# Kernel optimization log

Hardware: AMD Instinct MI355X
Metric: run time of the kernel (lower is better)

## Reference

```python
import jax, jax.numpy as jnp
import numpy as np
import math

EMB_DIM = 256
HEADS = 8
HEAD_DIM = EMB_DIM // HEADS
N_LAYERS = 6
GRID_H = 32
GRID_W = 32
SEQ = GRID_H * GRID_W
LN_EPS = 1e-5


def _layernorm(x, w, b):
    mu = jnp.mean(x, axis=-1, keepdims=True)
    var = jnp.mean(jnp.square(x - mu), axis=-1, keepdims=True)
    return (x - mu) * jax.lax.rsqrt(var + LN_EPS) * w + b


def _sinusoidal_table(num_pos, dim):
    inv_freq = 1.0 / (10000.0 ** (jnp.arange(0, dim, 2, dtype=jnp.float32) / dim))
    t = jnp.arange(num_pos, dtype=jnp.float32)
    sinusoid = t[:, None] * inv_freq[None, :]  # [P, dim/2]
    return jnp.concatenate([jnp.sin(sinusoid), jnp.cos(sinusoid)], axis=-1)  # [P, dim]


def _alibi_bias(num_heads, seq_len):
    # 2D Manhattan distances over the flattened grid (Two-slope-Alibi: factors = 1)
    xs, ys = jnp.meshgrid(jnp.arange(GRID_H), jnp.arange(GRID_W), indexing='ij')
    xf = xs.reshape(-1).astype(jnp.float32)
    yf = ys.reshape(-1).astype(jnp.float32)
    dist = jnp.abs(xf[:, None] - xf[None, :]) + jnp.abs(yf[:, None] - yf[None, :])
    dist = jnp.abs(dist[:seq_len, :seq_len])  # rpe_abs=True
    i = jnp.arange(num_heads, dtype=jnp.float32)
    slopes_l = -(2.0 ** (-(1.0 + i)))   # start_exponent=1, geometric ratio 1/2, times -1
    slopes_r = -(2.0 ** (-(0.5 + i)))   # start_exponent=0.5
    alibi_l = slopes_l[:, None, None] * dist[None]
    alibi_r = slopes_r[:, None, None] * dist[None]
    # triu + tril (diagonal dist = 0 so double-count is harmless)
    return jnp.triu(alibi_r) + jnp.tril(alibi_l)  # [H, S, S]


def reference(tokens, pos_ids, emb_table, input_weight, position_weight,
              ln1_w, ln1_b, ln2_w, ln2_b, w1, b1, w2, b2, lnf_w, lnf_b):
    B, S = tokens.shape
    # embeddings + sinusoidal positional embedding, mixed via weighted_sum_no_norm
    x_emb = emb_table[tokens]                                   # [B, S, D]
    pos_emb = _sinusoidal_table(SEQ, EMB_DIM)[pos_ids][None]    # [1, S, D]
    x = input_weight * x_emb + position_weight * pos_emb        # [B, S, D]

    bias = _alibi_bias(HEADS, S)[None]                          # [1, H, S, S]
    scale = 1.0 / math.sqrt(HEAD_DIM)

    for l in range(N_LAYERS):
        # --- attention: manual 2D-Alibi path (q = k = v = layernormed x; no projections) ---
        xn = _layernorm(x, ln1_w[l], ln1_b[l])
        qkv = xn.reshape(B, S, HEADS, HEAD_DIM).transpose(0, 2, 1, 3)  # [B, H, S, d]
        scores = jnp.einsum('bhsd,bhtd->bhst', qkv, qkv) * scale + bias
        attn = jax.nn.softmax(scores, axis=-1)
        out = jnp.einsum('bhst,bhtd->bhsd', attn, qkv)
        out = out.transpose(0, 2, 1, 3).reshape(B, S, EMB_DIM)
        x = x + out
        # --- MLP: Linear(D, 2*mlp_dim) -> GELU(exact) -> Linear(2*mlp_dim, D) ---
        xn = _layernorm(x, ln2_w[l], ln2_b[l])
        h = jax.nn.gelu(xn @ w1[l] + b1[l], approximate=False)
        x = x + (h @ w2[l] + b2[l])

    return _layernorm(x, lnf_w, lnf_b)


def setup_inputs() -> dict:
    key = jax.random.key(0)
    ks = jax.random.split(key, 8)
    B, S, D, L = 16, SEQ, EMB_DIM, N_LAYERS
    H2 = 2 * 512  # mlp hidden = mlp_dim * 2
    return {
        'tokens': jax.random.randint(ks[0], (B, S), 0, 16),
        'pos_ids': jnp.arange(S),
        'emb_table': jax.random.normal(ks[1], (16, D), dtype=jnp.float32),
        'input_weight': jnp.ones((1,), jnp.float32),
        'position_weight': jnp.ones((1,), jnp.float32),
        'ln1_w': jnp.ones((L, D), jnp.float32),
        'ln1_b': jnp.zeros((L, D), jnp.float32),
        'ln2_w': jnp.ones((L, D), jnp.float32),
        'ln2_b': jnp.zeros((L, D), jnp.float32),
        'w1': jax.random.normal(ks[2], (L, D, H2), dtype=jnp.float32) * (1.0 / np.sqrt(D)),
        'b1': jnp.zeros((L, H2), jnp.float32),
        'w2': jax.random.normal(ks[3], (L, H2, D), dtype=jnp.float32) * (1.0 / np.sqrt(H2)),
        'b2': jnp.zeros((L, D), jnp.float32),
        'lnf_w': jnp.ones((D,), jnp.float32),
        'lnf_b': jnp.zeros((D,), jnp.float32),
    }
```

## Files before the change

### kernel.cpp

```cpp
#include <hip/hip_runtime.h>
#include <hip/hip_bf16.h>
#include <math.h>

#define B_   16
#define S_   1024
#define D_   256
#define H_   8
#define HD_  32
#define L_   6
#define H2_  1024
#define LN_EPS 1e-5f
#define LOG2E_ 1.4426950408889634f
#define SCALE_ 0.17677669529663687f

typedef __attribute__((ext_vector_type(8))) short frag;
typedef __attribute__((ext_vector_type(4))) float f32x4;

#define MFMA(a, b, c) __builtin_amdgcn_mfma_f32_16x16x32_bf16((a), (b), (c), 0, 0, 0)

__device__ inline ushort bf16b(float f) {
    uint u = __builtin_bit_cast(uint, f);
    u += 0x7fff + ((u >> 16) & 1);
    return (ushort)(u >> 16);
}
__device__ inline uint cvt_pk_bf16(float lo, float hi) {
    uint r;
    asm("v_cvt_pk_bf16_f32 %0, %1, %2" : "=v"(r) : "v"(lo), "v"(hi));
    return r;
}
__device__ inline float exp2_raw(float x) {
    float r;
    asm("v_exp_f32 %0, %1" : "=v"(r) : "v"(x));
    return r;
}
__device__ __forceinline__ void gload16(const ushort* g, ushort* l) {
    __builtin_amdgcn_global_load_lds(
        (const __attribute__((address_space(1))) uint*)g,
        (__attribute__((address_space(3))) uint*)l, 16, 0, 0);
}

__global__ __launch_bounds__(256) void wtr_kernel(
    const float* __restrict__ in, ushort* __restrict__ out, int K, int N)
{
    __shared__ ushort Ts[32][36];
    in  += (size_t)blockIdx.z * K * N;
    out += (size_t)blockIdx.z * K * N;
    int n0 = blockIdx.x * 32, k0 = blockIdx.y * 32;
    int r = threadIdx.x >> 3, c4 = (threadIdx.x & 7) * 4;
    float4 f = *(const float4*)(in + (size_t)(k0 + r) * N + n0 + c4);
    Ts[r][c4 + 0] = bf16b(f.x);
    Ts[r][c4 + 1] = bf16b(f.y);
    Ts[r][c4 + 2] = bf16b(f.z);
    Ts[r][c4 + 3] = bf16b(f.w);
    __syncthreads();
    ushort4 o = { Ts[c4 + 0][r], Ts[c4 + 1][r], Ts[c4 + 2][r], Ts[c4 + 3][r] };
    *(ushort4*)(out + (size_t)(n0 + r) * K + k0 + c4) = o;
}

__global__ __launch_bounds__(256) void embed_kernel(
    const int* __restrict__ tokens, const int* __restrict__ pos_ids,
    const float* __restrict__ emb, const float* __restrict__ iwp,
    const float* __restrict__ pwp, float* __restrict__ X)
{
    int bs = blockIdx.x;
    int s = bs & (S_ - 1);
    int d = threadIdx.x;
    int tok = tokens[bs];
    float p = (float)pos_ids[s];
    int j = (d < 128) ? d : (d - 128);
    float invf = exp2f(-(float)j * (13.287712379549449f / 128.0f));
    float ang = p * invf;
    float pe = (d < 128) ? sinf(ang) : cosf(ang);
    X[(size_t)bs * D_ + d] = iwp[0] * emb[tok * D_ + d] + pwp[0] * pe;
}

template<int MODE>
__global__ __launch_bounds__(256) void ln_kernel(
    const float* __restrict__ X, const float* __restrict__ w,
    const float* __restrict__ b, void* __restrict__ outp)
{
    int row = blockIdx.x * 4 + (threadIdx.x >> 6);
    int lane = threadIdx.x & 63;
    const float4 v = *(const float4*)(X + (size_t)row * D_ + lane * 4);
    float s = v.x + v.y + v.z + v.w;
    #pragma unroll
    for (int m = 1; m < 64; m <<= 1) s += __shfl_xor(s, m, 64);
    float mu = s * (1.0f / 256.0f);
    float dx = v.x - mu, dy = v.y - mu, dz = v.z - mu, dw = v.w - mu;
    float vs = dx * dx + dy * dy + dz * dz + dw * dw;
    #pragma unroll
    for (int m = 1; m < 64; m <<= 1) vs += __shfl_xor(vs, m, 64);
    float inv = rsqrtf(vs * (1.0f / 256.0f) + LN_EPS);
    float4 wv = *(const float4*)(w + lane * 4);
    float4 bv = *(const float4*)(b + lane * 4);
    float o0 = dx * inv * wv.x + bv.x;
    float o1 = dy * inv * wv.y + bv.y;
    float o2 = dz * inv * wv.z + bv.z;
    float o3 = dw * inv * wv.w + bv.w;
    if constexpr (MODE == 0) {
        float4 o = { o0, o1, o2, o3 };
        *(float4*)((float*)outp + (size_t)row * D_ + lane * 4) = o;
    } else {
        ushort4 o = { bf16b(o0), bf16b(o1), bf16b(o2), bf16b(o3) };
        *(ushort4*)((ushort*)outp + (size_t)row * D_ + lane * 4) = o;
    }
}

__global__ __launch_bounds__(256) void lnv_kernel(
    const float* __restrict__ X, const float* __restrict__ w,
    const float* __restrict__ b, ushort* __restrict__ XNB,
    ushort* __restrict__ VTI)
{
    __shared__ ushort Ts[64][264];
    const int blk = blockIdx.x;
    const int bb = blk >> 4;
    const int sblk = (blk & 15) * 64;
    const int wv = threadIdx.x >> 6, lane = threadIdx.x & 63;

    #pragma unroll
    for (int p = 0; p < 16; ++p) {
        int srow = p * 4 + wv;
        int row = bb * S_ + sblk + srow;
        const float4 v = *(const float4*)(X + (size_t)row * D_ + lane * 4);
        float s = v.x + v.y + v.z + v.w;
        #pragma unroll
        for (int m = 1; m < 64; m <<= 1) s += __shfl_xor(s, m, 64);
        float mu = s * (1.0f / 256.0f);
        float dx = v.x - mu, dy = v.y - mu, dz = v.z - mu, dw = v.w - mu;
        float vs = dx * dx + dy * dy + dz * dz + dw * dw;
        #pragma unroll
        for (int m = 1; m < 64; m <<= 1) vs += __shfl_xor(vs, m, 64);
        float inv = rsqrtf(vs * (1.0f / 256.0f) + LN_EPS);
        float4 wvv = *(const float4*)(w + lane * 4);
        float4 bvv = *(const float4*)(b + lane * 4);
        ushort4 o = { bf16b(dx * inv * wvv.x + bvv.x),
                      bf16b(dy * inv * wvv.y + bvv.y),
                      bf16b(dz * inv * wvv.z + bvv.z),
                      bf16b(dw * inv * wvv.w + bvv.w) };
        int h = lane >> 3, dd = (lane & 7) * 4;
        *(ushort4*)(XNB + (((size_t)(bb * H_ + h) * S_ + sblk + srow) * HD_ + dd)) = o;
        *(ushort4*)&Ts[srow][lane * 4] = o;
    }
    __syncthreads();

    const int h = threadIdx.x >> 5, d = threadIdx.x & 31;
    const int hd = threadIdx.x;
    ushort* dst = VTI + ((size_t)(bb * H_ + h) * HD_ + d) * S_ + sblk;
    #pragma unroll
    for (int c8 = 0; c8 < 8; ++c8) {
        uint4 o;
        uint tmp[4];
        #pragma unroll
        for (int pair = 0; pair < 4; ++pair) {
            int c0 = c8 * 8 + pair * 2;
            int c1 = c0 + 1;
            int t0 = 16 * (((c0 >> 5) & 1) + 2 * ((c0 >> 2) & 1)) + 4 * ((c0 >> 3) & 3) + (c0 & 3);
            int t1 = 16 * (((c1 >> 5) & 1) + 2 * ((c1 >> 2) & 1)) + 4 * ((c1 >> 3) & 3) + (c1 & 3);
            tmp[pair] = (uint)Ts[t0][hd] | ((uint)Ts[t1][hd] << 16);
        }
        o.x = tmp[0]; o.y = tmp[1]; o.z = tmp[2]; o.w = tmp[3];
        *(uint4*)(dst + c8 * 8) = o;
    }
}

__global__ __launch_bounds__(256) void attn_kernel(
    const ushort* __restrict__ XNB, const ushort* __restrict__ VTI,
    float* __restrict__ X)
{
    __shared__ ushort Kl[2][2048];
    __shared__ ushort Vl[2][2048];

    const int bi = blockIdx.x;
    const int xcd = bi & 7, m = bi >> 3;
    const int bh = xcd * 16 + (m >> 3);
    const int bx = m & 7;
    const int b = bh >> 3, h = bh & 7;

    const ushort* __restrict__ base = XNB + (size_t)bh * (S_ * HD_);
    const ushort* __restrict__ vbase = VTI + (size_t)bh * (HD_ * S_);
    const int tid = threadIdx.x;
    const int w = tid >> 6, l = tid & 63, g = l >> 4, ll = l & 15;
    const int q0 = bx * 128 + w * 32;
    const int qgA = q0 + ll, qgB = q0 + 16 + ll;
    const int xq = q0 >> 5;
    const int yqA = ll, yqB = 16 + ll;

    const float C1 = SCALE_ * LOG2E_;
    frag qfA = *(const frag*)(base + (size_t)qgA * HD_ + g * 8);
    frag qfB = *(const frag*)(base + (size_t)qgB * HD_ + g * 8);
    #pragma unroll
    for (int i = 0; i < 8; ++i) {
        float fa = __builtin_bit_cast(float, ((uint)(ushort)qfA[i]) << 16);
        float fb = __builtin_bit_cast(float, ((uint)(ushort)qfB[i]) << 16);
        qfA[i] = (short)bf16b(fa * C1);
        qfB[i] = (short)bf16b(fb * C1);
    }

    const float slr = -exp2f(-(0.5f + (float)h)) * LOG2E_;
    const float sll = -exp2f(-(1.0f + (float)h)) * LOG2E_;
    const int itb = 2 * bx + (w >> 1);

    float dabs[4], d16m[4], d16p[4];
    #pragma unroll
    for (int r = 0; r < 4; ++r) {
        int del = ll - 4 * g - r;
        dabs[r] = (float)abs(del);
        d16m[r] = (float)(16 - del);
        d16p[r] = (float)(16 + del);
    }

    f32x4 o0A = {0,0,0,0}, o1A = {0,0,0,0}, osA = {0,0,0,0};
    f32x4 o0B = {0,0,0,0}, o1B = {0,0,0,0}, osB = {0,0,0,0};
    const f32x4 zc = {0,0,0,0};
    const short one_s = (short)0x3F80;
    const frag ones = { one_s, one_s, one_s, one_s, one_s, one_s, one_s, one_s };

    const ushort* ksrc = base  + (size_t)(16 * w + ll) * HD_ + g * 8;
    const ushort* vsrc = vbase + (size_t)((w >> 1) * 16 + ll) * S_ + (w & 1) * 32 + g * 8;
    const int dst = (w * 64 + l) * 8;

#define STAGE(NB, TILE)                                                       \
    gload16(ksrc + (size_t)(TILE) * 64 * HD_, &Kl[NB][dst]);                  \
    gload16(vsrc + (TILE) * 64,               &Vl[NB][dst]);

    STAGE(0, 0)
    __syncthreads();

#define EXACTR(r)                                                             \
  { int t0 = tb + 4 * g + (r);                                                \
    { int tg = t0;      int xt = tg >> 5, yt = tg & 31;                       \
      eA0[r] = exp2_raw(fmaf((tg > qgA) ? slr : sll,                          \
               (float)(abs(xq - xt) + abs(yqA - yt)), sa0[r]));               \
      eB0[r] = exp2_raw(fmaf((tg > qgB) ? slr : sll,                          \
               (float)(abs(xq - xt) + abs(yqB - yt)), sb0[r])); }             \
    { int tg = t0 + 16; int xt = tg >> 5, yt = tg & 31;                       \
      eA1[r] = exp2_raw(fmaf((tg > qgA) ? slr : sll,                          \
               (float)(abs(xq - xt) + abs(yqA - yt)), sa1[r]));               \
      eB1[r] = exp2_raw(fmaf((tg > qgB) ? slr : sll,                          \
               (float)(abs(xq - xt) + abs(yqB - yt)), sb1[r])); }             \
    { int tg = t0 + 32; int xt = tg >> 5, yt = tg & 31;                       \
      eA2[r] = exp2_raw(fmaf((tg > qgA) ? slr : sll,                          \
               (float)(abs(xq - xt) + abs(yqA - yt)), sa2[r]));               \
      eB2[r] = exp2_raw(fmaf((tg > qgB) ? slr : sll,                          \
               (float)(abs(xq - xt) + abs(yqB - yt)), sb2[r])); }             \
    { int tg = t0 + 48; int xt = tg >> 5, yt = tg & 31;                       \
      eA3[r] = exp2_raw(fmaf((tg > qgA) ? slr : sll,                          \
               (float)(abs(xq - xt) + abs(yqA - yt)), sa3[r]));               \
      eB3[r] = exp2_raw(fmaf((tg > qgB) ? slr : sll,                          \
               (float)(abs(xq - xt) + abs(yqB - yt)), sb3[r])); } }

#define FASTR(r)                                                              \
    eA0[r] = exp2_raw(fmaf(sl, dabs[r] + ax0, sa0[r]));                       \
    eA1[r] = exp2_raw(fmaf(sl, d16m[r] + ax0, sa1[r]));                       \
    eA2[r] = exp2_raw(fmaf(sl, dabs[r] + ax1, sa2[r]));                       \
    eA3[r] = exp2_raw(fmaf(sl, d16m[r] + ax1, sa3[r]));                       \
    eB0[r] = exp2_raw(fmaf(sl, d16p[r] + ax0, sb0[r]));                       \
    eB1[r] = exp2_raw(fmaf(sl, dabs[r] + ax0, sb1[r]));                       \
    eB2[r] = exp2_raw(fmaf(sl, d16p[r] + ax1, sb2[r]));                       \
    eB3[r] = exp2_raw(fmaf(sl, dabs[r] + ax1, sb3[r]));

    for (int it = 0; it < 16; ++it) {
        const int cur = it & 1, nxt = cur ^ 1;
        const int tb = it * 64;
        STAGE(nxt, (it + 1) & 15)

        frag K0 = *(const frag*)&Kl[cur][l * 8];
        frag K1 = *(const frag*)&Kl[cur][512 + l * 8];
        frag K2 = *(const frag*)&Kl[cur][1024 + l * 8];
        frag K3 = *(const frag*)&Kl[cur][1536 + l * 8];
        frag V0 = *(const frag*)&Vl[cur][l * 8];
        frag V2 = *(const frag*)&Vl[cur][512 + l * 8];
        frag V1 = *(const frag*)&Vl[cur][1024 + l * 8];
        frag V3 = *(const frag*)&Vl[cur][1536 + l * 8];

        f32x4 sa0 = MFMA(K0, qfA, zc);
        f32x4 sa1 = MFMA(K1, qfA, zc);
        f32x4 sa2 = MFMA(K2, qfA, zc);
        f32x4 sa3 = MFMA(K3, qfA, zc);
        f32x4 sb0 = MFMA(K0, qfB, zc);
        f32x4 sb1 = MFMA(K1, qfB, zc);
        f32x4 sb2 = MFMA(K2, qfB, zc);
        f32x4 sb3 = MFMA(K3, qfB, zc);

        f32x4 eA0, eA1, eA2, eA3, eB0, eB1, eB2, eB3;
        if (it == itb) {
            EXACTR(0) EXACTR(1) EXACTR(2) EXACTR(3)
        } else {
            const float sl = (it > itb) ? slr : sll;
            const float ax0 = (float)abs(xq - 2 * it);
            const float ax1 = (float)abs(xq - 2 * it - 1);
            FASTR(0) FASTR(1) FASTR(2) FASTR(3)
        }
        uint4 pa0 = { cvt_pk_bf16(eA0[0], eA0[1]), cvt_pk_bf16(eA0[2], eA0[3]),
                      cvt_pk_bf16(eA2[0], eA2[1]), cvt_pk_bf16(eA2[2], eA2[3]) };
        uint4 pa1 = { cvt_pk_bf16(eA1[0], eA1[1]), cvt_pk_bf16(eA1[2], eA1[3]),
                      cvt_pk_bf16(eA3[0], eA3[1]), cvt_pk_bf16(eA3[2], eA3[3]) };
        uint4 pb0 = { cvt_pk_bf16(eB0[0], eB0[1]), cvt_pk_bf16(eB0[2], eB0[3]),
                      cvt_pk_bf16(eB2[0], eB2[1]), cvt_pk_bf16(eB2[2], eB2[3]) };
        uint4 pb1 = { cvt_pk_bf16(eB1[0], eB1[1]), cvt_pk_bf16(eB1[2], eB1[3]),
                      cvt_pk_bf16(eB3[0], eB3[1]), cvt_pk_bf16(eB3[2], eB3[3]) };
        frag pfA0 = __builtin_bit_cast(frag, pa0);
        frag pfA1 = __builtin_bit_cast(frag, pa1);
        frag pfB0 = __builtin_bit_cast(frag, pb0);
        frag pfB1 = __builtin_bit_cast(frag, pb1);

        o0A = MFMA(pfA0, V0, o0A);  o1A = MFMA(pfA0, V1, o1A);
        osA = MFMA(pfA0, ones, osA);
        o0A = MFMA(pfA1, V2, o0A);  o1A = MFMA(pfA1, V3, o1A);
        osA = MFMA(pfA1, ones, osA);
        o0B = MFMA(pfB0, V0, o0B);  o1B = MFMA(pfB0, V1, o1B);
        osB = MFMA(pfB0, ones, osB);
        o0B = MFMA(pfB1, V2, o0B);  o1B = MFMA(pfB1, V3, o1B);
        osB = MFMA(pfB1, ones, osB);

        __syncthreads();
    }
#undef STAGE
#undef FASTR
#undef EXACTR

    #pragma unroll
    for (int r = 0; r < 4; ++r) {
        float invA = 1.0f / osA[r];
        float invB = 1.0f / osB[r];
        float* xpA = X + ((size_t)(b * S_ + q0 + g * 4 + r)) * D_ + h * HD_;
        float* xpB = X + ((size_t)(b * S_ + q0 + 16 + g * 4 + r)) * D_ + h * HD_;
        xpA[ll]      += o0A[r] * invA;
        xpA[16 + ll] += o1A[r] * invA;
        xpB[ll]      += o0B[r] * invB;
        xpB[16 + ll] += o1B[r] * invB;
    }
}

__global__ __launch_bounds__(256) void gemm1_kernel(
    const ushort* __restrict__ A, const ushort* __restrict__ Bt,
    const float* __restrict__ bias, ushort* __restrict__ Hout)
{
    __shared__ ushort As[128 * 32];
    __shared__ ushort Bs[128 * 32];
    const int bid = blockIdx.x;
    const int xcd = bid & 7, i = bid >> 3;
    const int row0 = (xcd * 16 + (i >> 3)) * 128;
    const int col0 = (i & 7) * 128;
    const int tid = threadIdx.x;
    const int w = tid >> 6, l = tid & 63, g = l >> 4, ll = l & 15;
    const int wm = w >> 1, wn = w & 1;

    const int srow = w * 32 + (l >> 2);
    const int scol = (l & 3) * 8;
    const ushort* ga = A  + (size_t)(row0 + srow) * 256 + scol;
    const ushort* gb = Bt + (size_t)(col0 + srow) * 256 + scol;
    ushort* lA = &As[w * 1024 + l * 8];
    ushort* lB = &Bs[w * 1024 + l * 8];

    f32x4 acc[4][4] = {};
    for (int k0 = 0; k0 < 256; k0 += 32) {
        __syncthreads();
        gload16(ga + k0,            lA);
        gload16(ga + k0 + 16 * 256, lA + 512);
        gload16(gb + k0,            lB);
        gload16(gb + k0 + 16 * 256, lB + 512);
        __syncthreads();
        frag af[4], bfr[4];
        #pragma unroll
        for (int mb = 0; mb < 4; ++mb)
            af[mb] = *(const frag*)&As[(wm * 64 + mb * 16 + ll) * 32 + g * 8];
        #pragma unroll
        for (int nb = 0; nb < 4; ++nb)
            bfr[nb] = *(const frag*)&Bs[(wn * 64 + nb * 16 + ll) * 32 + g * 8];
        #pragma unroll
        for (int mb = 0; mb < 4; ++mb)
            #pragma unroll
            for (int nb = 0; nb < 4; ++nb)
                acc[mb][nb] = MFMA(af[mb], bfr[nb], acc[mb][nb]);
    }

    #pragma unroll
    for (int nb = 0; nb < 4; ++nb) {
        int col = col0 + wn * 64 + nb * 16 + ll;
        float bv = bias[col];
        #pragma unroll
        for (int mb = 0; mb < 4; ++mb) {
            #pragma unroll
            for (int r = 0; r < 4; ++r) {
                int row = row0 + wm * 64 + mb * 16 + g * 4 + r;
                float v = acc[mb][nb][r] + bv;
                float u2 = 1.5957691216f * v + 0.0713548162f * (v * v * v);
                float e = exp2_raw(u2 * LOG2E_);
                float rr = __builtin_amdgcn_rcpf(e + 1.0f);
                float gl = v - v * rr;
                Hout[(size_t)row * 1024 + col] = bf16b(gl);
            }
        }
    }
}

__global__ __launch_bounds__(256) void gemm2_kernel(
    const ushort* __restrict__ A, const ushort* __restrict__ Bt,
    const float* __restrict__ bias, float* __restrict__ X)
{
    __shared__ ushort As[128 * 32];
    __shared__ ushort Bs[64 * 32];
    const int bid = blockIdx.x;
    const int xcd = bid & 7, i = bid >> 3;
    const int row0 = (xcd * 16 + (i >> 2)) * 128;
    const int col0 = (i & 3) * 64;
    const int tid = threadIdx.x;
    const int w = tid >> 6, l = tid & 63, g = l >> 4, ll = l & 15;

    const int srow = w * 32 + (l >> 2);
    const int scol = (l & 3) * 8;
    const ushort* ga = A  + (size_t)(row0 + srow) * 1024 + scol;
    const ushort* gb = Bt + (size_t)(col0 + w * 16 + (l >> 2)) * 1024 + scol;
    ushort* lA = &As[w * 1024 + l * 8];
    ushort* lB = &Bs[w * 512 + l * 8];

    f32x4 acc[2][4] = {};
    for (int k0 = 0; k0 < 1024; k0 += 32) {
        __syncthreads();
        gload16(ga + k0,             lA);
        gload16(ga + k0 + 16 * 1024, lA + 512);
        gload16(gb + k0,             lB);
        __syncthreads();
        frag af[2], bfr[4];
        #pragma unroll
        for (int mb = 0; mb < 2; ++mb)
            af[mb] = *(const frag*)&As[(w * 32 + mb * 16 + ll) * 32 + g * 8];
        #pragma unroll
        for (int nb = 0; nb < 4; ++nb)
            bfr[nb] = *(const frag*)&Bs[(nb * 16 + ll) * 32 + g * 8];
        #pragma unroll
        for (int mb = 0; mb < 2; ++mb)
            #pragma unroll
            for (int nb = 0; nb < 4; ++nb)
                acc[mb][nb] = MFMA(af[mb], bfr[nb], acc[mb][nb]);
    }

    #pragma unroll
    for (int nb = 0; nb < 4; ++nb) {
        int col = col0 + nb * 16 + ll;
        float bv = bias[col];
        #pragma unroll
        for (int mb = 0; mb < 2; ++mb) {
            #pragma unroll
            for (int r = 0; r < 4; ++r) {
                int row = row0 + w * 32 + mb * 16 + g * 4 + r;
                float* xp = X + (size_t)row * 256 + col;
                *xp += acc[mb][nb][r] + bv;
            }
        }
    }
}

extern "C" void kernel_launch(void* const* d_in, const int* in_sizes, int n_in,
                              void* d_out, int out_size, void* d_ws, size_t ws_size,
                              hipStream_t stream)
{
    const int*   tokens  = (const int*)d_in[0];
    const int*   pos_ids = (const int*)d_in[1];
    const float* emb     = (const float*)d_in[2];
    const float* iw      = (const float*)d_in[3];
    const float* pw      = (const float*)d_in[4];
    const float* ln1w    = (const float*)d_in[5];
    const float* ln1b    = (const float*)d_in[6];
    const float* ln2w    = (const float*)d_in[7];
    const float* ln2b    = (const float*)d_in[8];
    const float* w1      = (const float*)d_in[9];
    const float* b1      = (const float*)d_in[10];
    const float* w2      = (const float*)d_in[11];
    const float* b2      = (const float*)d_in[12];
    const float* lnfw    = (const float*)d_in[13];
    const float* lnfb    = (const float*)d_in[14];

    float* x = (float*)d_out;
    char* ws = (char*)d_ws;
    ushort* xn   = (ushort*)ws;
    ushort* vti  = (ushort*)(ws + 8388608);
    ushort* hbuf = (ushort*)(ws + 16777216);
    ushort* w1t  = (ushort*)(ws + 50331648);
    ushort* w2t  = (ushort*)(ws + 53477376);

    wtr_kernel<<<dim3(32, 8, L_), 256, 0, stream>>>(w1, w1t, 256, 1024);
    wtr_kernel<<<dim3(8, 32, L_), 256, 0, stream>>>(w2, w2t, 1024, 256);

    embed_kernel<<<B_ * S_, 256, 0, stream>>>(tokens, pos_ids, emb, iw, pw, x);

    for (int l = 0; l < L_; l++) {
        lnv_kernel<<<(B_ * S_) / 64, 256, 0, stream>>>(
            x, ln1w + l * D_, ln1b + l * D_, xn, vti);
        attn_kernel<<<(S_ / 128) * B_ * H_, 256, 0, stream>>>(xn, vti, x);
        ln_kernel<2><<<(B_ * S_) / 4, 256, 0, stream>>>(x, ln2w + l * D_, ln2b + l * D_, xn);
        gemm1_kernel<<<1024, 256, 0, stream>>>(
            xn, w1t + (size_t)l * D_ * H2_, b1 + (size_t)l * H2_, hbuf);
        gemm2_kernel<<<512, 256, 0, stream>>>(
            hbuf, w2t + (size_t)l * H2_ * D_, b2 + (size_t)l * D_, x);
    }
    ln_kernel<0><<<(B_ * S_) / 4, 256, 0, stream>>>(x, lnfw, lnfb, x);
}
```

Baseline: 642.5 us.

## Double-buffer LDS tiles in both MLP GEMM kernels to overlap loads with MFMA

Both MLP GEMM kernels now keep two LDS stages and issue the global-to-LDS loads for the next K-slice before running the MFMAs on the current slice. This drops one of the two barriers per iteration and is meant to hide global load latency behind compute. In exchange LDS use doubles, which may lower occupancy, and the last iteration does a redundant wrap-around load of slice zero. Correctness depends on the gload16 direct-to-LDS path being complete by the single barrier at the end of each iteration.

```diff
diff --git a/kernel.cpp b/kernel.cpp
--- a/kernel.cpp
+++ b/kernel.cpp
@@ -336,8 +336,8 @@
     const ushort* __restrict__ A, const ushort* __restrict__ Bt,
     const float* __restrict__ bias, ushort* __restrict__ Hout)
 {
-    __shared__ ushort As[128 * 32];
-    __shared__ ushort Bs[128 * 32];
+    __shared__ ushort As[2][128 * 32];
+    __shared__ ushort Bs[2][128 * 32];
     const int bid = blockIdx.x;
     const int xcd = bid & 7, i = bid >> 3;
     const int row0 = (xcd * 16 + (i >> 3)) * 128;
@@ -350,30 +350,36 @@
     const int scol = (l & 3) * 8;
     const ushort* ga = A  + (size_t)(row0 + srow) * 256 + scol;
     const ushort* gb = Bt + (size_t)(col0 + srow) * 256 + scol;
-    ushort* lA = &As[w * 1024 + l * 8];
-    ushort* lB = &Bs[w * 1024 + l * 8];
+    const int dst = w * 1024 + l * 8;
+
+#define G1STAGE(NB, K0)                                                       \
+    gload16(ga + (K0),            &As[NB][dst]);                              \
+    gload16(ga + (K0) + 16 * 256, &As[NB][dst + 512]);                        \
+    gload16(gb + (K0),            &Bs[NB][dst]);                              \
+    gload16(gb + (K0) + 16 * 256, &Bs[NB][dst + 512]);
+
+    G1STAGE(0, 0)
+    __syncthreads();
 
     f32x4 acc[4][4] = {};
-    for (int k0 = 0; k0 < 256; k0 += 32) {
-        __syncthreads();
-        gload16(ga + k0,            lA);
-        gload16(ga + k0 + 16 * 256, lA + 512);
-        gload16(gb + k0,            lB);
-        gload16(gb + k0 + 16 * 256, lB + 512);
-        __syncthreads();
+    for (int it = 0; it < 8; ++it) {
+        const int cur = it & 1, nxt = cur ^ 1;
+        G1STAGE(nxt, ((it + 1) & 7) * 32)
         frag af[4], bfr[4];
         #pragma unroll
         for (int mb = 0; mb < 4; ++mb)
-            af[mb] = *(const frag*)&As[(wm * 64 + mb * 16 + ll) * 32 + g * 8];
+            af[mb] = *(const frag*)&As[cur][(wm * 64 + mb * 16 + ll) * 32 + g * 8];
         #pragma unroll
         for (int nb = 0; nb < 4; ++nb)
-            bfr[nb] = *(const frag*)&Bs[(wn * 64 + nb * 16 + ll) * 32 + g * 8];
+            bfr[nb] = *(const frag*)&Bs[cur][(wn * 64 + nb * 16 + ll) * 32 + g * 8];
         #pragma unroll
         for (int mb = 0; mb < 4; ++mb)
             #pragma unroll
             for (int nb = 0; nb < 4; ++nb)
                 acc[mb][nb] = MFMA(af[mb], bfr[nb], acc[mb][nb]);
-    }
+        __syncthreads();
+    }
+#undef G1STAGE
 
     #pragma unroll
     for (int nb = 0; nb < 4; ++nb) {
@@ -399,8 +405,8 @@
     const ushort* __restrict__ A, const ushort* __restrict__ Bt,
     const float* __restrict__ bias, float* __restrict__ X)
 {
-    __shared__ ushort As[128 * 32];
-    __shared__ ushort Bs[64 * 32];
+    __shared__ ushort As[2][128 * 32];
+    __shared__ ushort Bs[2][64 * 32];
     const int bid = blockIdx.x;
     const int xcd = bid & 7, i = bid >> 3;
     const int row0 = (xcd * 16 + (i >> 2)) * 128;
@@ -412,29 +418,36 @@
     const int scol = (l & 3) * 8;
     const ushort* ga = A  + (size_t)(row0 + srow) * 1024 + scol;
     const ushort* gb = Bt + (size_t)(col0 + w * 16 + (l >> 2)) * 1024 + scol;
-    ushort* lA = &As[w * 1024 + l * 8];
-    ushort* lB = &Bs[w * 512 + l * 8];
+    const int dstA = w * 1024 + l * 8;
+    const int dstB = w * 512 + l * 8;
+
+#define G2STAGE(NB, K0)                                                       \
+    gload16(ga + (K0),             &As[NB][dstA]);                            \
+    gload16(ga + (K0) + 16 * 1024, &As[NB][dstA + 512]);                      \
+    gload16(gb + (K0),             &Bs[NB][dstB]);
+
+    G2STAGE(0, 0)
+    __syncthreads();
 
     f32x4 acc[2][4] = {};
-    for (int k0 = 0; k0 < 1024; k0 += 32) {
-        __syncthreads();
-        gload16(ga + k0,             lA);
-        gload16(ga + k0 + 16 * 1024, lA + 512);
-        gload16(gb + k0,             lB);
-        __syncthreads();
+    for (int it = 0; it < 32; ++it) {
+        const int cur = it & 1, nxt = cur ^ 1;
+        G2STAGE(nxt, ((it + 1) & 31) * 32)
         frag af[2], bfr[4];
         #pragma unroll
         for (int mb = 0; mb < 2; ++mb)
-            af[mb] = *(const frag*)&As[(w * 32 + mb * 16 + ll) * 32 + g * 8];
+            af[mb] = *(const frag*)&As[cur][(w * 32 + mb * 16 + ll) * 32 + g * 8];
         #pragma unroll
         for (int nb = 0; nb < 4; ++nb)
-            bfr[nb] = *(const frag*)&Bs[(nb * 16 + ll) * 32 + g * 8];
+            bfr[nb] = *(const frag*)&Bs[cur][(nb * 16 + ll) * 32 + g * 8];
         #pragma unroll
         for (int mb = 0; mb < 2; ++mb)
             #pragma unroll
             for (int nb = 0; nb < 4; ++nb)
                 acc[mb][nb] = MFMA(af[mb], bfr[nb], acc[mb][nb]);
-    }
+        __syncthreads();
+    }
+#undef G2STAGE
 
     #pragma unroll
     for (int nb = 0; nb < 4; ++nb) {
```

After: 674.8 us. +5.0%, slower.

## Fuse LayerNorm, MLP up-projection with GELU, and down-projection into one kernel

Applied to the files above, without the earlier changes.

Replaces the separate ln2, gemm1 and gemm2 kernels with a single mlp_kernel. Each block handles 32 rows: it layernorms them into swizzled LDS, computes the 1024-wide GELU hidden activations into LDS, then does the down-projection and residual add. This removes the global round-trip of the 32 MB hidden buffer and two launches per layer. In exchange, weight B-fragments are read directly from global/L2 without LDS tiling. The 80 KB of LDS per block also limits occupancy.

```diff
diff --git a/kernel.cpp b/kernel.cpp
--- a/kernel.cpp
+++ b/kernel.cpp
@@ -74,10 +74,9 @@
     X[(size_t)bs * D_ + d] = iwp[0] * emb[tok * D_ + d] + pwp[0] * pe;
 }
 
-template<int MODE>
-__global__ __launch_bounds__(256) void ln_kernel(
+__global__ __launch_bounds__(256) void lnf_kernel(
     const float* __restrict__ X, const float* __restrict__ w,
-    const float* __restrict__ b, void* __restrict__ outp)
+    const float* __restrict__ b, float* __restrict__ outp)
 {
     int row = blockIdx.x * 4 + (threadIdx.x >> 6);
     int lane = threadIdx.x & 63;
@@ -93,17 +92,12 @@
     float inv = rsqrtf(vs * (1.0f / 256.0f) + LN_EPS);
     float4 wv = *(const float4*)(w + lane * 4);
     float4 bv = *(const float4*)(b + lane * 4);
-    float o0 = dx * inv * wv.x + bv.x;
-    float o1 = dy * inv * wv.y + bv.y;
-    float o2 = dz * inv * wv.z + bv.z;
-    float o3 = dw * inv * wv.w + bv.w;
-    if constexpr (MODE == 0) {
-        float4 o = { o0, o1, o2, o3 };
-        *(float4*)((float*)outp + (size_t)row * D_ + lane * 4) = o;
-    } else {
-        ushort4 o = { bf16b(o0), bf16b(o1), bf16b(o2), bf16b(o3) };
-        *(ushort4*)((ushort*)outp + (size_t)row * D_ + lane * 4) = o;
-    }
+    float4 o;
+    o.x = dx * inv * wv.x + bv.x;
+    o.y = dy * inv * wv.y + bv.y;
+    o.z = dz * inv * wv.z + bv.z;
+    o.w = dw * inv * wv.w + bv.w;
+    *(float4*)(outp + (size_t)row * D_ + lane * 4) = o;
 }
 
 __global__ __launch_bounds__(256) void lnv_kernel(
@@ -332,121 +326,112 @@
     }
 }
 
-__global__ __launch_bounds__(256) void gemm1_kernel(
-    const ushort* __restrict__ A, const ushort* __restrict__ Bt,
-    const float* __restrict__ bias, ushort* __restrict__ Hout)
-{
-    __shared__ ushort As[128 * 32];
-    __shared__ ushort Bs[128 * 32];
-    const int bid = blockIdx.x;
-    const int xcd = bid & 7, i = bid >> 3;
-    const int row0 = (xcd * 16 + (i >> 3)) * 128;
-    const int col0 = (i & 7) * 128;
+__global__ __launch_bounds__(256) void mlp_kernel(
+    float* __restrict__ X, const float* __restrict__ lw,
+    const float* __restrict__ lb, const ushort* __restrict__ W1t,
+    const float* __restrict__ b1, const ushort* __restrict__ W2t,
+    const float* __restrict__ b2)
+{
+    __shared__ ushort xnt[32 * 256];
+    __shared__ ushort hbf[32 * 1024];
+    const int row0 = blockIdx.x * 32;
     const int tid = threadIdx.x;
     const int w = tid >> 6, l = tid & 63, g = l >> 4, ll = l & 15;
-    const int wm = w >> 1, wn = w & 1;
-
-    const int srow = w * 32 + (l >> 2);
-    const int scol = (l & 3) * 8;
-    const ushort* ga = A  + (size_t)(row0 + srow) * 256 + scol;
-    const ushort* gb = Bt + (size_t)(col0 + srow) * 256 + scol;
-    ushort* lA = &As[w * 1024 + l * 8];
-    ushort* lB = &Bs[w * 1024 + l * 8];
-
-    f32x4 acc[4][4] = {};
-    for (int k0 = 0; k0 < 256; k0 += 32) {
-        __syncthreads();
-        gload16(ga + k0,            lA);
-        gload16(ga + k0 + 16 * 256, lA + 512);
-        gload16(gb + k0,            lB);
-        gload16(gb + k0 + 16 * 256, lB + 512);
-        __syncthreads();
-        frag af[4], bfr[4];
-        #pragma unroll
-        for (int mb = 0; mb < 4; ++mb)
-            af[mb] = *(const frag*)&As[(wm * 64 + mb * 16 + ll) * 32 + g * 8];
-        #pragma unroll
-        for (int nb = 0; nb < 4; ++nb)
-            bfr[nb] = *(const frag*)&Bs[(wn * 64 + nb * 16 + ll) * 32 + g * 8];
-        #pragma unroll
-        for (int mb = 0; mb < 4; ++mb)
-            #pragma unroll
-            for (int nb = 0; nb < 4; ++nb)
-                acc[mb][nb] = MFMA(af[mb], bfr[nb], acc[mb][nb]);
-    }
-
-    #pragma unroll
-    for (int nb = 0; nb < 4; ++nb) {
-        int col = col0 + wn * 64 + nb * 16 + ll;
-        float bv = bias[col];
-        #pragma unroll
-        for (int mb = 0; mb < 4; ++mb) {
+
+    const float4 wv4 = *(const float4*)(lw + l * 4);
+    const float4 bv4 = *(const float4*)(lb + l * 4);
+    #pragma unroll
+    for (int p = 0; p < 8; ++p) {
+        int r = w * 8 + p;
+        const float4 v = *(const float4*)(X + (size_t)(row0 + r) * D_ + l * 4);
+        float s = v.x + v.y + v.z + v.w;
+        #pragma unroll
+        for (int m = 1; m < 64; m <<= 1) s += __shfl_xor(s, m, 64);
+        float mu = s * (1.0f / 256.0f);
+        float dx = v.x - mu, dy = v.y - mu, dz = v.z - mu, dw = v.w - mu;
+        float vs = dx * dx + dy * dy + dz * dz + dw * dw;
+        #pragma unroll
+        for (int m = 1; m < 64; m <<= 1) vs += __shfl_xor(vs, m, 64);
+        float inv = rsqrtf(vs * (1.0f / 256.0f) + LN_EPS);
+        ushort4 o = { bf16b(dx * inv * wv4.x + bv4.x),
+                      bf16b(dy * inv * wv4.y + bv4.y),
+                      bf16b(dz * inv * wv4.z + bv4.z),
+                      bf16b(dw * inv * wv4.w + bv4.w) };
+        *(ushort4*)&xnt[r * 256 + ((l * 4) ^ ((r & 7) << 3))] = o;
+    }
+    __syncthreads();
+
+    const int cbase = w * 256;
+    frag af[2][8];
+    #pragma unroll
+    for (int m = 0; m < 2; ++m) {
+        int row = m * 16 + ll;
+        int sw = (row & 7) << 3;
+        #pragma unroll
+        for (int ks = 0; ks < 8; ++ks)
+            af[m][ks] = *(const frag*)&xnt[row * 256 + ((ks * 32 + g * 8) ^ sw)];
+    }
+    const f32x4 zc = {0, 0, 0, 0};
+    #pragma unroll 2
+    for (int nf = 0; nf < 16; ++nf) {
+        const int col = cbase + nf * 16 + ll;
+        const float bv = b1[col];
+        const ushort* wp = W1t + (size_t)col * 256 + g * 8;
+        frag bfr[8];
+        #pragma unroll
+        for (int ks = 0; ks < 8; ++ks)
+            bfr[ks] = *(const frag*)(wp + ks * 32);
+        f32x4 a0 = zc, a1 = zc;
+        #pragma unroll
+        for (int ks = 0; ks < 8; ++ks) {
+            a0 = MFMA(af[0][ks], bfr[ks], a0);
+            a1 = MFMA(af[1][ks], bfr[ks], a1);
+        }
+        const int swc = cbase + nf * 16 + ll;
+        #pragma unroll
+        for (int r = 0; r < 4; ++r) {
+            int row = g * 4 + r;
+            float v = a0[r] + bv;
+            float u2 = 1.5957691216f * v + 0.0713548162f * (v * v * v);
+            float e = exp2_raw(u2 * LOG2E_);
+            float gl = v - v * __builtin_amdgcn_rcpf(e + 1.0f);
+            hbf[row * 1024 + (swc ^ ((row & 7) << 3))] = bf16b(gl);
+            int row2 = 16 + row;
+            float v2 = a1[r] + bv;
+            float u22 = 1.5957691216f * v2 + 0.0713548162f * (v2 * v2 * v2);
+            float e2 = exp2_raw(u22 * LOG2E_);
+            float gl2 = v2 - v2 * __builtin_amdgcn_rcpf(e2 + 1.0f);
+            hbf[row2 * 1024 + (swc ^ ((row2 & 7) << 3))] = bf16b(gl2);
+        }
+    }
+    __syncthreads();
+
+    const int obase = w * 64;
+    const ushort* w2p = W2t + (size_t)(obase + ll) * 1024 + g * 8;
+    const int swll = (ll & 7) << 3;
+    f32x4 acc[2][4] = {};
+    #pragma unroll 4
+    for (int ks = 0; ks < 32; ++ks) {
+        frag a0 = *(const frag*)&hbf[ll * 1024 + ((ks * 32 + g * 8) ^ swll)];
+        frag a1 = *(const frag*)&hbf[(16 + ll) * 1024 + ((ks * 32 + g * 8) ^ swll)];
+        #pragma unroll
+        for (int nf = 0; nf < 4; ++nf) {
+            frag bfr = *(const frag*)(w2p + (size_t)(nf * 16) * 1024 + ks * 32);
+            acc[0][nf] = MFMA(a0, bfr, acc[0][nf]);
+            acc[1][nf] = MFMA(a1, bfr, acc[1][nf]);
+        }
+    }
+    #pragma unroll
+    for (int nf = 0; nf < 4; ++nf) {
+        int col = obase + nf * 16 + ll;
+        float bv = b2[col];
+        #pragma unroll
+        for (int m = 0; m < 2; ++m) {
             #pragma unroll
             for (int r = 0; r < 4; ++r) {
-                int row = row0 + wm * 64 + mb * 16 + g * 4 + r;
-                float v = acc[mb][nb][r] + bv;
-                float u2 = 1.5957691216f * v + 0.0713548162f * (v * v * v);
-                float e = exp2_raw(u2 * LOG2E_);
-                float rr = __builtin_amdgcn_rcpf(e + 1.0f);
-                float gl = v - v * rr;
-                Hout[(size_t)row * 1024 + col] = bf16b(gl);
-            }
-        }
-    }
-}
-
-__global__ __launch_bounds__(256) void gemm2_kernel(
-    const ushort* __restrict__ A, const ushort* __restrict__ Bt,
-    const float* __restrict__ bias, float* __restrict__ X)
-{
-    __shared__ ushort As[128 * 32];
-    __shared__ ushort Bs[64 * 32];
-    const int bid = blockIdx.x;
-    const int xcd = bid & 7, i = bid >> 3;
-    const int row0 = (xcd * 16 + (i >> 2)) * 128;
-    const int col0 = (i & 3) * 64;
-    const int tid = threadIdx.x;
-    const int w = tid >> 6, l = tid & 63, g = l >> 4, ll = l & 15;
-
-    const int srow = w * 32 + (l >> 2);
-    const int scol = (l & 3) * 8;
-    const ushort* ga = A  + (size_t)(row0 + srow) * 1024 + scol;
-    const ushort* gb = Bt + (size_t)(col0 + w * 16 + (l >> 2)) * 1024 + scol;
-    ushort* lA = &As[w * 1024 + l * 8];
-    ushort* lB = &Bs[w * 512 + l * 8];
-
-    f32x4 acc[2][4] = {};
-    for (int k0 = 0; k0 < 1024; k0 += 32) {
-        __syncthreads();
-        gload16(ga + k0,             lA);
-        gload16(ga + k0 + 16 * 1024, lA + 512);
-        gload16(gb + k0,             lB);
-        __syncthreads();
-        frag af[2], bfr[4];
-        #pragma unroll
-        for (int mb = 0; mb < 2; ++mb)
-            af[mb] = *(const frag*)&As[(w * 32 + mb * 16 + ll) * 32 + g * 8];
-        #pragma unroll
-        for (int nb = 0; nb < 4; ++nb)
-            bfr[nb] = *(const frag*)&Bs[(nb * 16 + ll) * 32 + g * 8];
-        #pragma unroll
-        for (int mb = 0; mb < 2; ++mb)
-            #pragma unroll
-            for (int nb = 0; nb < 4; ++nb)
-                acc[mb][nb] = MFMA(af[mb], bfr[nb], acc[mb][nb]);
-    }
-
-    #pragma unroll
-    for (int nb = 0; nb < 4; ++nb) {
-        int col = col0 + nb * 16 + ll;
-        float bv = bias[col];
-        #pragma unroll
-        for (int mb = 0; mb < 2; ++mb) {
-            #pragma unroll
-            for (int r = 0; r < 4; ++r) {
-                int row = row0 + w * 32 + mb * 16 + g * 4 + r;
-                float* xp = X + (size_t)row * 256 + col;
-                *xp += acc[mb][nb][r] + bv;
+                int row = row0 + m * 16 + g * 4 + r;
+                float* xp = X + (size_t)row * D_ + col;
+                *xp += acc[m][nf][r] + bv;
             }
         }
     }
@@ -476,7 +461,6 @@
     char* ws = (char*)d_ws;
     ushort* xn   = (ushort*)ws;
     ushort* vti  = (ushort*)(ws + 8388608);
-    ushort* hbuf = (ushort*)(ws + 16777216);
     ushort* w1t  = (ushort*)(ws + 50331648);
     ushort* w2t  = (ushort*)(ws + 53477376);
 
@@ -489,11 +473,10 @@
         lnv_kernel<<<(B_ * S_) / 64, 256, 0, stream>>>(
             x, ln1w + l * D_, ln1b + l * D_, xn, vti);
         attn_kernel<<<(S_ / 128) * B_ * H_, 256, 0, stream>>>(xn, vti, x);
-        ln_kernel<2><<<(B_ * S_) / 4, 256, 0, stream>>>(x, ln2w + l * D_, ln2b + l * D_, xn);
-        gemm1_kernel<<<1024, 256, 0, stream>>>(
-            xn, w1t + (size_t)l * D_ * H2_, b1 + (size_t)l * H2_, hbuf);
-        gemm2_kernel<<<512, 256, 0, stream>>>(
-            hbuf, w2t + (size_t)l * H2_ * D_, b2 + (size_t)l * D_, x);
-    }
-    ln_kernel<0><<<(B_ * S_) / 4, 256, 0, stream>>>(x, lnfw, lnfb, x);
-}
+        mlp_kernel<<<(B_ * S_) / 32, 256, 0, stream>>>(
+            x, ln2w + l * D_, ln2b + l * D_,
+            w1t + (size_t)l * D_ * H2_, b1 + (size_t)l * H2_,
+            w2t + (size_t)l * H2_ * D_, b2 + (size_t)l * D_);
+    }
+    lnf_kernel<<<(B_ * S_) / 4, 256, 0, stream>>>(x, lnfw, lnfb, x);
+}
```

Measured after the change: 750.5 us. 16.8% more time.
